# Performance work log

Hardware: AMD Instinct MI355X
Metric: run time of the kernel (lower is better)

Reference implementation:

```python
import jax, jax.numpy as jnp
import numpy as np

EMBED_DIM = 2048
NUM_HEADS = 16
HEAD_DIM = EMBED_DIM // NUM_HEADS
B, T = 4, 2048


def setup_inputs() -> dict:
    key = jax.random.key(0)
    ks = jax.random.split(key, 9)
    s = 1.0 / np.sqrt(EMBED_DIM)
    x = jax.random.normal(ks[0], (B, T, EMBED_DIM), dtype=jnp.float32)
    Wq = jax.random.normal(ks[1], (EMBED_DIM, EMBED_DIM), dtype=jnp.float32) * s
    bq = jnp.zeros((EMBED_DIM,), dtype=jnp.float32)
    Wk = jax.random.normal(ks[2], (EMBED_DIM, EMBED_DIM), dtype=jnp.float32) * s
    bk = jnp.zeros((EMBED_DIM,), dtype=jnp.float32)
    Wv = jax.random.normal(ks[3], (EMBED_DIM, EMBED_DIM), dtype=jnp.float32) * s
    bv = jnp.zeros((EMBED_DIM,), dtype=jnp.float32)
    Wo = jax.random.normal(ks[4], (EMBED_DIM, EMBED_DIM), dtype=jnp.float32) * s
    bo = jnp.zeros((EMBED_DIM,), dtype=jnp.float32)
    return {"x": x, "Wq": Wq, "bq": bq, "Wk": Wk, "bk": bk,
            "Wv": Wv, "bv": bv, "Wo": Wo, "bo": bo}


def reference(x, Wq, bq, Wk, bk, Wv, bv, Wo, bo):
    Bb, Tt, C = x.shape
    H, D = NUM_HEADS, C // NUM_HEADS
    # QKV projections (Linear: x @ W.T + b), reshape to [B, H, T, D]
    q = (jnp.einsum('btc,oc->bto', x, Wq) + bq).reshape(Bb, Tt, H, D).transpose(0, 2, 1, 3)
    k = (jnp.einsum('btc,oc->bto', x, Wk) + bk).reshape(Bb, Tt, H, D).transpose(0, 2, 1, 3)
    v = (jnp.einsum('btc,oc->bto', x, Wv) + bv).reshape(Bb, Tt, H, D).transpose(0, 2, 1, 3)
    logits = jnp.einsum('bhqd,bhkd->bhqk', q, k) / jnp.sqrt(jnp.float32(D))
    causal = jnp.triu(jnp.ones((Tt, Tt), dtype=bool), 1)  # True above diagonal
    logits = jnp.where(causal, -jnp.inf, logits)
    attn = jax.nn.softmax(logits, axis=-1)
    out = jnp.einsum('bhqk,bhkd->bhqd', attn, v)  # [B, H, T, D]
    out = out.transpose(0, 2, 1, 3).reshape(Bb, Tt, C)
    y = jnp.einsum('btc,oc->bto', out, Wo) + bo
    return y
```

## Files before the change

kernel.cpp:

```cpp
#include <hip/hip_runtime.h>
#include <hip/hip_bf16.h>
#include <cstdint>
#include <cstddef>

typedef __attribute__((ext_vector_type(8))) short short8;
typedef __attribute__((ext_vector_type(4))) short short4_;
typedef __attribute__((ext_vector_type(4))) float floatx4;
typedef __attribute__((ext_vector_type(4))) unsigned short ushort4_;

#define MFMA16(a, b, c) __builtin_amdgcn_mfma_f32_16x16x32_bf16((a), (b), (c), 0, 0, 0)

__device__ __forceinline__ unsigned short f2bf(float f) {
  __hip_bfloat16 h = __float2bfloat16(f);
  return *reinterpret_cast<unsigned short*>(&h);
}

__device__ __forceinline__ void gl_lds16(const void* g, void* lds) {
  __builtin_amdgcn_global_load_lds(
      (const __attribute__((address_space(1))) void*)g,
      (__attribute__((address_space(3))) void*)lds, 16, 0, 0);
}

__global__ void cast_f32_bf16(const float* __restrict__ in, __hip_bfloat16* __restrict__ out) {
  const int i = (blockIdx.x * 256 + threadIdx.x) * 4;
  const float4 v = *reinterpret_cast<const float4*>(in + i);
  ushort4_ o = { f2bf(v.x), f2bf(v.y), f2bf(v.z), f2bf(v.w) };
  *reinterpret_cast<ushort4_*>(out + i) = o;
}

template <int MODE>
__global__ __launch_bounds__(512, 2)
void gemm256(const __hip_bfloat16* __restrict__ Ap, const __hip_bfloat16* __restrict__ Bp,
             const float* __restrict__ bias, void* __restrict__ Cout,
             int M, int N, int K) {
  __shared__ __align__(16) __hip_bfloat16 SA[4][256 * 32];
  __shared__ __align__(16) __hip_bfloat16 SB[4][256 * 32];

  const int tid = threadIdx.x;
  const int wid = tid >> 6, lane = tid & 63;
  const int wr = wid >> 2, wc = wid & 3;
  const int g = lane >> 4, c16 = lane & 15;

  const int swzb = (blockIdx.x & 7) * 32 + (blockIdx.x >> 3);
  const int bm = swzb >> 3, bn = swzb & 7;

  const int srow = lane >> 2;
  const int slog = (lane & 3) ^ ((lane >> 3) & 3);
  const int swz = c16 * 32 + (g ^ ((c16 >> 1) & 3)) * 8;

  floatx4 acc[8][4] = {};

  auto stage = [&](int kt) {
    const int kb = kt * 32;
    const int slot = kt & 3;
#pragma unroll
    for (int i = 0; i < 2; ++i) {
      const int rbase = i * 128 + wid * 16;
      gl_lds16(Ap + (size_t)(bm * 256 + rbase + srow) * K + kb + slog * 8,
               SA[slot] + rbase * 32);
      gl_lds16(Bp + (size_t)(bn * 256 + rbase + srow) * K + kb + slog * 8,
               SB[slot] + rbase * 32);
    }
  };

  auto compute = [&](int slot) {
    const __hip_bfloat16* sa = SA[slot];
    const __hip_bfloat16* sb = SB[slot];
    short8 af[8], bf[4];
#pragma unroll
    for (int m = 0; m < 8; ++m)
      af[m] = *reinterpret_cast<const short8*>(sa + wr * 4096 + m * 512 + swz);
#pragma unroll
    for (int n = 0; n < 4; ++n)
      bf[n] = *reinterpret_cast<const short8*>(sb + wc * 2048 + n * 512 + swz);
    __builtin_amdgcn_s_setprio(1);
#pragma unroll
    for (int m = 0; m < 8; ++m)
#pragma unroll
      for (int n = 0; n < 4; ++n)
        acc[m][n] = MFMA16(af[m], bf[n], acc[m][n]);
    __builtin_amdgcn_s_setprio(0);
  };

  const int nkt = K >> 5;
  stage(0); stage(1); stage(2);

  for (int kt = 0; kt < nkt - 3; ++kt) {
    asm volatile("s_waitcnt vmcnt(8)" ::: "memory");
    __builtin_amdgcn_s_barrier();
    stage(kt + 3);
    compute(kt & 3);
  }
  asm volatile("s_waitcnt vmcnt(8)" ::: "memory");
  __builtin_amdgcn_s_barrier();
  compute((nkt - 3) & 3);
  asm volatile("s_waitcnt vmcnt(4)" ::: "memory");
  __builtin_amdgcn_s_barrier();
  compute((nkt - 2) & 3);
  asm volatile("s_waitcnt vmcnt(0)" ::: "memory");
  __builtin_amdgcn_s_barrier();
  compute((nkt - 1) & 3);

#pragma unroll
  for (int n = 0; n < 4; ++n) {
    const int colg = bn * 256 + wc * 64 + n * 16 + c16;
    const float bv = bias[colg];
#pragma unroll
    for (int m = 0; m < 8; ++m) {
      const int rowg = bm * 256 + wr * 128 + m * 16 + g * 4;
      if (MODE == 0) {
        __hip_bfloat16* C = (__hip_bfloat16*)Cout;
#pragma unroll
        for (int j = 0; j < 4; ++j)
          C[(size_t)(rowg + j) * N + colg] = __float2bfloat16(acc[m][n][j] + bv);
      } else if (MODE == 1) {
        __hip_bfloat16* C = (__hip_bfloat16*)Cout;
        const int bb = rowg >> 11, t0 = rowg & 2047;
        ushort4_ pk = { f2bf(acc[m][n][0] + bv), f2bf(acc[m][n][1] + bv),
                        f2bf(acc[m][n][2] + bv), f2bf(acc[m][n][3] + bv) };
        *reinterpret_cast<ushort4_*>(C + ((size_t)bb * 2048 + colg) * 2048 + t0) = pk;
      } else {
        float* C = (float*)Cout;
#pragma unroll
        for (int j = 0; j < 4; ++j)
          C[(size_t)(rowg + j) * N + colg] = acc[m][n][j] + bv;
      }
    }
  }
}

__global__ __launch_bounds__(256, 2)
void attn_fwd4(const __hip_bfloat16* __restrict__ Q, const __hip_bfloat16* __restrict__ K,
               const __hip_bfloat16* __restrict__ Vt, __hip_bfloat16* __restrict__ ctx) {
  constexpr int T = 2048, C = 2048, D = 128;
  __shared__ __align__(16) __hip_bfloat16 Ks[64][136];
  __shared__ __align__(16) __hip_bfloat16 Vs[128][64];
  __shared__ __align__(16) __hip_bfloat16 Pl[4][32][64];

  const int tid = threadIdx.x;
  const int w = tid >> 6, lane = tid & 63;
  const int g = lane >> 4, c16 = lane & 15;

  const int bid = blockIdx.x;
  const int swz = (bid & 7) * 128 + (bid >> 3);
  const int bh = swz >> 4, qb = 15 - (swz & 15);
  const int b = bh >> 4, h = bh & 15;
  const int wq = qb * 128 + w * 32;

  const __hip_bfloat16* Qh = Q + (size_t)b * T * C + h * D;
  const __hip_bfloat16* Kh = K + (size_t)b * T * C + h * D;
  const __hip_bfloat16* Vh = Vt + (size_t)bh * D * T;

  short8 qf[2][4];
#pragma unroll
  for (int m = 0; m < 2; ++m)
#pragma unroll
    for (int kk = 0; kk < 4; ++kk)
      qf[m][kk] = *reinterpret_cast<const short8*>(Qh + (size_t)(wq + m * 16 + c16) * C + kk * 32 + g * 8);

  floatx4 acc[2][8] = {};
  float mrow[2] = {-INFINITY, -INFINITY};
  float lrow[2] = {0.f, 0.f};

  const float scale = 0.08838834764831845f;
  const int krow = tid >> 4, kcol = (tid & 15) * 8;
  const int vrow = tid >> 3;
  const int vslot = (tid & 7) ^ (vrow & 7);
  const int vgcol = (tid & 7) * 8;

  short8 kr[4], vr[4];
  auto gloadK = [&](int kb) {
#pragma unroll
    for (int p = 0; p < 4; ++p)
      kr[p] = *reinterpret_cast<const short8*>(Kh + (size_t)(kb + p * 16 + krow) * C + kcol);
  };
  auto gloadV = [&](int kb) {
#pragma unroll
    for (int p = 0; p < 4; ++p)
      vr[p] = *reinterpret_cast<const short8*>(Vh + (size_t)(p * 32 + vrow) * T + kb + vgcol);
  };

  __hip_bfloat16 (*Pq)[64] = Pl[w];
  const int nkt = qb * 2 + 2;
  gloadK(0);
  gloadV(0);

  for (int kt = 0; kt < nkt; ++kt) {
    const int kb = kt * 64;
    __syncthreads();
#pragma unroll
    for (int p = 0; p < 4; ++p)
      *reinterpret_cast<short8*>(&Ks[p * 16 + krow][kcol]) = kr[p];
#pragma unroll
    for (int p = 0; p < 4; ++p)
      *reinterpret_cast<short8*>(&Vs[p * 32 + vrow][vslot * 8]) = vr[p];
    __syncthreads();

    const bool hasnext = (kt + 1 < nkt);
    const bool part = (kb <= wq + 31);
    if (hasnext) gloadK(kb + 64);

    if (part) {
      const bool needmask = (kb + 63 > wq);
      floatx4 s[2][4] = {};
      __builtin_amdgcn_s_setprio(1);
#pragma unroll
      for (int n = 0; n < 4; ++n)
#pragma unroll
        for (int kk = 0; kk < 4; ++kk) {
          short8 kf = *reinterpret_cast<const short8*>(&Ks[n * 16 + c16][kk * 32 + g * 8]);
          s[0][n] = MFMA16(kf, qf[0][kk], s[0][n]);
          s[1][n] = MFMA16(kf, qf[1][kk], s[1][n]);
        }
      __builtin_amdgcn_s_setprio(0);
      float vmax[2];
#pragma unroll
      for (int m = 0; m < 2; ++m) {
        const int q = wq + m * 16 + c16;
        float vm = -INFINITY;
#pragma unroll
        for (int n = 0; n < 4; ++n)
#pragma unroll
          for (int j = 0; j < 4; ++j) {
            float a = s[m][n][j] * scale;
            if (needmask && (kb + n * 16 + g * 4 + j > q)) a = -INFINITY;
            s[m][n][j] = a;
            vm = fmaxf(vm, a);
          }
        vm = fmaxf(vm, __shfl_xor(vm, 16));
        vm = fmaxf(vm, __shfl_xor(vm, 32));
        vmax[m] = vm;
      }
      const float grow = fmaxf(vmax[0] - mrow[0], vmax[1] - mrow[1]);
      const bool nore = __all(grow <= 8.0f);
#pragma unroll
      for (int m = 0; m < 2; ++m) {
        const float mn = nore ? mrow[m] : fmaxf(mrow[m], vmax[m]);
        float rs = 0.f;
#pragma unroll
        for (int n = 0; n < 4; ++n) {
          float p0 = __expf(s[m][n][0] - mn), p1 = __expf(s[m][n][1] - mn);
          float p2 = __expf(s[m][n][2] - mn), p3 = __expf(s[m][n][3] - mn);
          rs += (p0 + p1) + (p2 + p3);
          ushort4_ pk = { f2bf(p0), f2bf(p1), f2bf(p2), f2bf(p3) };
          *reinterpret_cast<ushort4_*>(&Pq[m * 16 + c16][((4 * n + g) ^ c16) * 4]) = pk;
        }
        rs += __shfl_xor(rs, 16);
        rs += __shfl_xor(rs, 32);
        if (nore) {
          lrow[m] += rs;
        } else {
          const float sc = __expf(mrow[m] - mn);
          lrow[m] = lrow[m] * sc + rs;
          mrow[m] = mn;
#pragma unroll
          for (int dt = 0; dt < 8; ++dt)
#pragma unroll
            for (int j = 0; j < 4; ++j) acc[m][dt][j] *= sc;
        }
      }
    }
    if (hasnext) gloadV(kb + 64);
    if (part) {
      short8 pb[2][2];
#pragma unroll
      for (int m = 0; m < 2; ++m)
#pragma unroll
        for (int ks = 0; ks < 2; ++ks) {
          short4_ lo = *reinterpret_cast<const short4_*>(&Pq[m * 16 + c16][((8 * ks + 2 * g) ^ c16) * 4]);
          short4_ hi = *reinterpret_cast<const short4_*>(&Pq[m * 16 + c16][((8 * ks + 2 * g + 1) ^ c16) * 4]);
          short8 r;
          r[0] = lo[0]; r[1] = lo[1]; r[2] = lo[2]; r[3] = lo[3];
          r[4] = hi[0]; r[5] = hi[1]; r[6] = hi[2]; r[7] = hi[3];
          pb[m][ks] = r;
        }
      __builtin_amdgcn_s_setprio(1);
#pragma unroll
      for (int dt = 0; dt < 8; ++dt)
#pragma unroll
        for (int ks = 0; ks < 2; ++ks) {
          const int pslot = ((ks * 4 + g) ^ (c16 & 7)) * 8;
          short8 vf = *reinterpret_cast<const short8*>(&Vs[dt * 16 + c16][pslot]);
          acc[0][dt] = MFMA16(vf, pb[0][ks], acc[0][dt]);
          acc[1][dt] = MFMA16(vf, pb[1][ks], acc[1][dt]);
        }
      __builtin_amdgcn_s_setprio(0);
    }
  }

#pragma unroll
  for (int m = 0; m < 2; ++m) {
    const float inv = 1.0f / lrow[m];
    const size_t row = (size_t)b * T + wq + m * 16 + c16;
#pragma unroll
    for (int dt = 0; dt < 8; ++dt) {
      ushort4_ o = { f2bf(acc[m][dt][0] * inv), f2bf(acc[m][dt][1] * inv),
                     f2bf(acc[m][dt][2] * inv), f2bf(acc[m][dt][3] * inv) };
      *reinterpret_cast<ushort4_*>(ctx + row * C + h * D + dt * 16 + g * 4) = o;
    }
  }
}

extern "C" void kernel_launch(void* const* d_in, const int* in_sizes, int n_in,
                              void* d_out, int out_size, void* d_ws, size_t ws_size,
                              hipStream_t stream) {
  const float* x  = (const float*)d_in[0];
  const float* Wq = (const float*)d_in[1];
  const float* bq = (const float*)d_in[2];
  const float* Wk = (const float*)d_in[3];
  const float* bk = (const float*)d_in[4];
  const float* Wv = (const float*)d_in[5];
  const float* bv = (const float*)d_in[6];
  const float* Wo = (const float*)d_in[7];
  const float* bo = (const float*)d_in[8];

  const int M = 8192, N = 2048, K = 2048;
  const size_t MB = 1u << 20;
  char* ws = (char*)d_ws;
  __hip_bfloat16* xb  = (__hip_bfloat16*)(ws);
  __hip_bfloat16* wqb = (__hip_bfloat16*)(ws + 32 * MB);
  __hip_bfloat16* wkb = (__hip_bfloat16*)(ws + 40 * MB);
  __hip_bfloat16* wvb = (__hip_bfloat16*)(ws + 48 * MB);
  __hip_bfloat16* wob = (__hip_bfloat16*)(ws + 56 * MB);
  __hip_bfloat16* Qb  = (__hip_bfloat16*)(ws + 64 * MB);
  __hip_bfloat16* Kb  = (__hip_bfloat16*)(ws + 96 * MB);
  __hip_bfloat16* Vtb = (__hip_bfloat16*)(ws + 128 * MB);
  if (ws_size < 160 * MB) return;

  cast_f32_bf16<<<(M * N) / 1024, 256, 0, stream>>>(x, xb);
  cast_f32_bf16<<<(N * K) / 1024, 256, 0, stream>>>(Wq, wqb);
  cast_f32_bf16<<<(N * K) / 1024, 256, 0, stream>>>(Wk, wkb);
  cast_f32_bf16<<<(N * K) / 1024, 256, 0, stream>>>(Wv, wvb);
  cast_f32_bf16<<<(N * K) / 1024, 256, 0, stream>>>(Wo, wob);

  const dim3 gg((M / 256) * (N / 256));
  gemm256<0><<<gg, 512, 0, stream>>>(xb, wqb, bq, Qb, M, N, K);
  gemm256<0><<<gg, 512, 0, stream>>>(xb, wkb, bk, Kb, M, N, K);
  gemm256<1><<<gg, 512, 0, stream>>>(xb, wvb, bv, Vtb, M, N, K);

  attn_fwd4<<<64 * 16, 256, 0, stream>>>(Qb, Kb, Vtb, xb);

  gemm256<2><<<gg, 512, 0, stream>>>(xb, wob, bo, d_out, M, N, K);
}
```

Before: 534.2 us.

## Fuse cast kernels, swizzle K tile, shrink P buffer, raise attention occupancy

Merges the five float-to-bf16 cast launches into one grid that dispatches by block index. In attention, K tiles get an XOR-swizzled LDS layout in place of padding. Each wave's P scratch is halved by reading P back right after writing it for each m, and softmax uses exp2 with log2e folded into the scale. The launch bound rises to 4 blocks per SM to increase occupancy, which risks register spills and the P reuse adds intra-wave ordering hazards.

```diff
diff --git a/kernel.cpp b/kernel.cpp
--- a/kernel.cpp
+++ b/kernel.cpp
@@ -21,11 +21,25 @@
       (__attribute__((address_space(3))) void*)lds, 16, 0, 0);
 }
 
-__global__ void cast_f32_bf16(const float* __restrict__ in, __hip_bfloat16* __restrict__ out) {
-  const int i = (blockIdx.x * 256 + threadIdx.x) * 4;
-  const float4 v = *reinterpret_cast<const float4*>(in + i);
+__global__ void cast5_f32_bf16(const float* __restrict__ x, const float* __restrict__ wq,
+                               const float* __restrict__ wk, const float* __restrict__ wv,
+                               const float* __restrict__ wo,
+                               __hip_bfloat16* __restrict__ xb, __hip_bfloat16* __restrict__ wqb,
+                               __hip_bfloat16* __restrict__ wkb, __hip_bfloat16* __restrict__ wvb,
+                               __hip_bfloat16* __restrict__ wob) {
+  const int bid = blockIdx.x;
+  const float* src;
+  __hip_bfloat16* dst;
+  int base;
+  if (bid < 16384)      { src = x;  dst = xb;  base = bid; }
+  else if (bid < 20480) { src = wq; dst = wqb; base = bid - 16384; }
+  else if (bid < 24576) { src = wk; dst = wkb; base = bid - 20480; }
+  else if (bid < 28672) { src = wv; dst = wvb; base = bid - 24576; }
+  else                  { src = wo; dst = wob; base = bid - 28672; }
+  const int i = base * 1024 + threadIdx.x * 4;
+  const float4 v = *reinterpret_cast<const float4*>(src + i);
   ushort4_ o = { f2bf(v.x), f2bf(v.y), f2bf(v.z), f2bf(v.w) };
-  *reinterpret_cast<ushort4_*>(out + i) = o;
+  *reinterpret_cast<ushort4_*>(dst + i) = o;
 }
 
 template <int MODE>
@@ -129,13 +143,13 @@
   }
 }
 
-__global__ __launch_bounds__(256, 2)
-void attn_fwd4(const __hip_bfloat16* __restrict__ Q, const __hip_bfloat16* __restrict__ K,
+__global__ __launch_bounds__(256, 4)
+void attn_fwd5(const __hip_bfloat16* __restrict__ Q, const __hip_bfloat16* __restrict__ K,
                const __hip_bfloat16* __restrict__ Vt, __hip_bfloat16* __restrict__ ctx) {
   constexpr int T = 2048, C = 2048, D = 128;
-  __shared__ __align__(16) __hip_bfloat16 Ks[64][136];
-  __shared__ __align__(16) __hip_bfloat16 Vs[128][64];
-  __shared__ __align__(16) __hip_bfloat16 Pl[4][32][64];
+  __shared__ __align__(16) __hip_bfloat16 Ks[64 * 128];
+  __shared__ __align__(16) __hip_bfloat16 Vs[128 * 64];
+  __shared__ __align__(16) __hip_bfloat16 Pl[4][16 * 64];
 
   const int tid = threadIdx.x;
   const int w = tid >> 6, lane = tid & 63;
@@ -162,17 +176,19 @@
   float mrow[2] = {-INFINITY, -INFINITY};
   float lrow[2] = {0.f, 0.f};
 
-  const float scale = 0.08838834764831845f;
-  const int krow = tid >> 4, kcol = (tid & 15) * 8;
+  const float scale2 = 0.12751744f;
+  const int krow = tid >> 4;
+  const int kslot = (tid & 15) ^ (krow & 7);
   const int vrow = tid >> 3;
   const int vslot = (tid & 7) ^ (vrow & 7);
   const int vgcol = (tid & 7) * 8;
+  const int kgcol = (tid & 15) * 8;
 
   short8 kr[4], vr[4];
   auto gloadK = [&](int kb) {
 #pragma unroll
     for (int p = 0; p < 4; ++p)
-      kr[p] = *reinterpret_cast<const short8*>(Kh + (size_t)(kb + p * 16 + krow) * C + kcol);
+      kr[p] = *reinterpret_cast<const short8*>(Kh + (size_t)(kb + p * 16 + krow) * C + kgcol);
   };
   auto gloadV = [&](int kb) {
 #pragma unroll
@@ -180,7 +196,7 @@
       vr[p] = *reinterpret_cast<const short8*>(Vh + (size_t)(p * 32 + vrow) * T + kb + vgcol);
   };
 
-  __hip_bfloat16 (*Pq)[64] = Pl[w];
+  __hip_bfloat16* Pq = Pl[w];
   const int nkt = qb * 2 + 2;
   gloadK(0);
   gloadV(0);
@@ -190,16 +206,17 @@
     __syncthreads();
 #pragma unroll
     for (int p = 0; p < 4; ++p)
-      *reinterpret_cast<short8*>(&Ks[p * 16 + krow][kcol]) = kr[p];
+      *reinterpret_cast<short8*>(&Ks[(p * 16 + krow) * 128 + kslot * 8]) = kr[p];
 #pragma unroll
     for (int p = 0; p < 4; ++p)
-      *reinterpret_cast<short8*>(&Vs[p * 32 + vrow][vslot * 8]) = vr[p];
+      *reinterpret_cast<short8*>(&Vs[(p * 32 + vrow) * 64 + vslot * 8]) = vr[p];
     __syncthreads();
 
     const bool hasnext = (kt + 1 < nkt);
     const bool part = (kb <= wq + 31);
     if (hasnext) gloadK(kb + 64);
 
+    short8 pb[2][2];
     if (part) {
       const bool needmask = (kb + 63 > wq);
       floatx4 s[2][4] = {};
@@ -208,7 +225,8 @@
       for (int n = 0; n < 4; ++n)
 #pragma unroll
         for (int kk = 0; kk < 4; ++kk) {
-          short8 kf = *reinterpret_cast<const short8*>(&Ks[n * 16 + c16][kk * 32 + g * 8]);
+          short8 kf = *reinterpret_cast<const short8*>(
+              &Ks[(n * 16 + c16) * 128 + (((kk * 4 + g) ^ (c16 & 7)) * 8)]);
           s[0][n] = MFMA16(kf, qf[0][kk], s[0][n]);
           s[1][n] = MFMA16(kf, qf[1][kk], s[1][n]);
         }
@@ -222,7 +240,7 @@
         for (int n = 0; n < 4; ++n)
 #pragma unroll
           for (int j = 0; j < 4; ++j) {
-            float a = s[m][n][j] * scale;
+            float a = s[m][n][j] * scale2;
             if (needmask && (kb + n * 16 + g * 4 + j > q)) a = -INFINITY;
             s[m][n][j] = a;
             vm = fmaxf(vm, a);
@@ -239,18 +257,18 @@
         float rs = 0.f;
 #pragma unroll
         for (int n = 0; n < 4; ++n) {
-          float p0 = __expf(s[m][n][0] - mn), p1 = __expf(s[m][n][1] - mn);
-          float p2 = __expf(s[m][n][2] - mn), p3 = __expf(s[m][n][3] - mn);
+          float p0 = exp2f(s[m][n][0] - mn), p1 = exp2f(s[m][n][1] - mn);
+          float p2 = exp2f(s[m][n][2] - mn), p3 = exp2f(s[m][n][3] - mn);
           rs += (p0 + p1) + (p2 + p3);
           ushort4_ pk = { f2bf(p0), f2bf(p1), f2bf(p2), f2bf(p3) };
-          *reinterpret_cast<ushort4_*>(&Pq[m * 16 + c16][((4 * n + g) ^ c16) * 4]) = pk;
+          *reinterpret_cast<ushort4_*>(&Pq[c16 * 64 + (((4 * n + g) ^ c16) * 4)]) = pk;
         }
         rs += __shfl_xor(rs, 16);
         rs += __shfl_xor(rs, 32);
         if (nore) {
           lrow[m] += rs;
         } else {
-          const float sc = __expf(mrow[m] - mn);
+          const float sc = exp2f(mrow[m] - mn);
           lrow[m] = lrow[m] * sc + rs;
           mrow[m] = mn;
 #pragma unroll
@@ -258,29 +276,26 @@
 #pragma unroll
             for (int j = 0; j < 4; ++j) acc[m][dt][j] *= sc;
         }
-      }
-    }
-    if (hasnext) gloadV(kb + 64);
-    if (part) {
-      short8 pb[2][2];
-#pragma unroll
-      for (int m = 0; m < 2; ++m)
 #pragma unroll
         for (int ks = 0; ks < 2; ++ks) {
-          short4_ lo = *reinterpret_cast<const short4_*>(&Pq[m * 16 + c16][((8 * ks + 2 * g) ^ c16) * 4]);
-          short4_ hi = *reinterpret_cast<const short4_*>(&Pq[m * 16 + c16][((8 * ks + 2 * g + 1) ^ c16) * 4]);
+          short4_ lo = *reinterpret_cast<const short4_*>(&Pq[c16 * 64 + (((8 * ks + 2 * g) ^ c16) * 4)]);
+          short4_ hi = *reinterpret_cast<const short4_*>(&Pq[c16 * 64 + (((8 * ks + 2 * g + 1) ^ c16) * 4)]);
           short8 r;
           r[0] = lo[0]; r[1] = lo[1]; r[2] = lo[2]; r[3] = lo[3];
           r[4] = hi[0]; r[5] = hi[1]; r[6] = hi[2]; r[7] = hi[3];
           pb[m][ks] = r;
         }
+      }
+    }
+    if (hasnext) gloadV(kb + 64);
+    if (part) {
       __builtin_amdgcn_s_setprio(1);
 #pragma unroll
       for (int dt = 0; dt < 8; ++dt)
 #pragma unroll
         for (int ks = 0; ks < 2; ++ks) {
           const int pslot = ((ks * 4 + g) ^ (c16 & 7)) * 8;
-          short8 vf = *reinterpret_cast<const short8*>(&Vs[dt * 16 + c16][pslot]);
+          short8 vf = *reinterpret_cast<const short8*>(&Vs[(dt * 16 + c16) * 64 + pslot]);
           acc[0][dt] = MFMA16(vf, pb[0][ks], acc[0][dt]);
           acc[1][dt] = MFMA16(vf, pb[1][ks], acc[1][dt]);
         }
@@ -327,18 +342,14 @@
   __hip_bfloat16* Vtb = (__hip_bfloat16*)(ws + 128 * MB);
   if (ws_size < 160 * MB) return;
 
-  cast_f32_bf16<<<(M * N) / 1024, 256, 0, stream>>>(x, xb);
-  cast_f32_bf16<<<(N * K) / 1024, 256, 0, stream>>>(Wq, wqb);
-  cast_f32_bf16<<<(N * K) / 1024, 256, 0, stream>>>(Wk, wkb);
-  cast_f32_bf16<<<(N * K) / 1024, 256, 0, stream>>>(Wv, wvb);
-  cast_f32_bf16<<<(N * K) / 1024, 256, 0, stream>>>(Wo, wob);
+  cast5_f32_bf16<<<32768, 256, 0, stream>>>(x, Wq, Wk, Wv, Wo, xb, wqb, wkb, wvb, wob);
 
   const dim3 gg((M / 256) * (N / 256));
   gemm256<0><<<gg, 512, 0, stream>>>(xb, wqb, bq, Qb, M, N, K);
   gemm256<0><<<gg, 512, 0, stream>>>(xb, wkb, bk, Kb, M, N, K);
   gemm256<1><<<gg, 512, 0, stream>>>(xb, wvb, bv, Vtb, M, N, K);
 
-  attn_fwd4<<<64 * 16, 256, 0, stream>>>(Qb, Kb, Vtb, xb);
+  attn_fwd5<<<64 * 16, 256, 0, stream>>>(Qb, Kb, Vtb, xb);
 
   gemm256<2><<<gg, 512, 0, stream>>>(xb, wob, bo, d_out, M, N, K);
 }
```

Result: slower. 922.9 us (+72.8%).
